# Kernel tuning notes

Hardware: AMD Instinct MI355X
Metric: run time of the kernel (lower is better)

Reference implementation:

```python
import jax, jax.numpy as jnp
import numpy as np
from jax.scipy.special import logsumexp


def _mixture_log_cdf(x, pi, mu, s):
    # x: [B,C,H,W]; pi,mu,s: [B,C,H,W,K]. log CDF of mixture of logistics.
    z = (x[..., None] - mu) * jnp.exp(-s)
    return logsumexp(jax.nn.log_softmax(pi, axis=-1) + jax.nn.log_sigmoid(z), axis=-1)


def _mixture_log_pdf(x, pi, mu, s):
    z = (x[..., None] - mu) * jnp.exp(-s)
    log_p = z - s - 2.0 * jax.nn.softplus(z)  # logistic log-density per component
    return logsumexp(jax.nn.log_softmax(pi, axis=-1) + log_p, axis=-1)


def setup_inputs() -> dict:
    key = jax.random.key(0)
    ks = jax.random.split(key, 8)
    B, C, H, W, K = 32, 8, 64, 64, 16
    shp = (B, C, H, W)
    mshp = (B, C, H, W, K)
    return {
        "x_change": jax.random.normal(ks[0], shp, jnp.float32),
        "x_id": jax.random.normal(ks[1], shp, jnp.float32),
        "sldj": jnp.zeros((B,), jnp.float32),
        "a": 0.1 * jax.random.normal(ks[2], shp, jnp.float32),
        "b": 0.1 * jax.random.normal(ks[3], shp, jnp.float32),
        "pi": jax.random.normal(ks[4], mshp, jnp.float32),
        "mu": jax.random.normal(ks[5], mshp, jnp.float32),
        "s": 0.1 * jax.random.normal(ks[6], mshp, jnp.float32),
    }


def reference(x_change, x_id, sldj, a, b, pi, mu, s):
    B = x_change.shape[0]
    # forward (reverse=False) Flow++ MixLogCDF coupling
    log_cdf = _mixture_log_cdf(x_change, pi, mu, s)  # [B,C,H,W], values <= 0
    u = jnp.exp(log_cdf)                             # CDF in (0,1)
    # sigmoid inverse (logit) with log-det: z = log(u) - log(1-u); ldj = -log(u) - log(1-u)
    out = log_cdf - jnp.log1p(-u)
    scale_ldj = -log_cdf - jnp.log1p(-u)
    out = (out + b) * jnp.exp(a)
    logistic_ldj = _mixture_log_pdf(x_change, pi, mu, s)
    sldj = sldj + jnp.sum((logistic_ldj + scale_ldj + a).reshape(B, -1), axis=-1)
    return out, x_id, sldj
```

## Files before the change

kernel.cpp:

```cpp
#include <hip/hip_runtime.h>
#include <math.h>

#define KCOMP 16
#define CHW 32768

__global__ void init_sldj_kernel(const float* __restrict__ sldj,
                                 float* __restrict__ out_sldj, int B) {
    int i = blockIdx.x * blockDim.x + threadIdx.x;
    if (i < B) out_sldj[i] = sldj[i];
}

__global__ __launch_bounds__(256) void coupling_kernel(
    const float* __restrict__ x_change, const float* __restrict__ x_id,
    const float* __restrict__ a, const float* __restrict__ b,
    const float* __restrict__ pi, const float* __restrict__ mu,
    const float* __restrict__ s, float* __restrict__ out, int N) {
    const int i = blockIdx.x * blockDim.x + threadIdx.x;
    float ldj_term = 0.0f;
    if (i < N) {
        const float x = x_change[i];

        float p[KCOMP], m[KCOMP], sv[KCOMP];
        const size_t base = (size_t)i * KCOMP;
        const float4* pv = (const float4*)(pi + base);
        const float4* mv = (const float4*)(mu + base);
        const float4* svv = (const float4*)(s + base);
#pragma unroll
        for (int c = 0; c < 4; ++c) {
            float4 t0 = pv[c];
            p[4 * c + 0] = t0.x; p[4 * c + 1] = t0.y; p[4 * c + 2] = t0.z; p[4 * c + 3] = t0.w;
            float4 t1 = mv[c];
            m[4 * c + 0] = t1.x; m[4 * c + 1] = t1.y; m[4 * c + 2] = t1.z; m[4 * c + 3] = t1.w;
            float4 t2 = svv[c];
            sv[4 * c + 0] = t2.x; sv[4 * c + 1] = t2.y; sv[4 * c + 2] = t2.z; sv[4 * c + 3] = t2.w;
        }

        float pmax = p[0];
#pragma unroll
        for (int k = 1; k < KCOMP; ++k) pmax = fmaxf(pmax, p[k]);
        float psum = 0.0f;
#pragma unroll
        for (int k = 0; k < KCOMP; ++k) psum += __expf(p[k] - pmax);
        const float lse_pi = pmax + __logf(psum);

        float t[KCOMP], q[KCOMP];
        float mt = -1e30f, mq = -1e30f;
#pragma unroll
        for (int k = 0; k < KCOMP; ++k) {
            const float lp = p[k] - lse_pi;
            const float sk = sv[k];
            const float z = (x - m[k]) * __expf(-sk);
            const float az = fabsf(z);
            const float l1 = __logf(1.0f + __expf(-az));
            const float ls = fminf(z, 0.0f) - l1;
            const float sp = fmaxf(z, 0.0f) + l1;
            const float logp = z - sk - 2.0f * sp;
            t[k] = lp + ls;
            q[k] = lp + logp;
            mt = fmaxf(mt, t[k]);
            mq = fmaxf(mq, q[k]);
        }
        float st = 0.0f, sq = 0.0f;
#pragma unroll
        for (int k = 0; k < KCOMP; ++k) {
            st += __expf(t[k] - mt);
            sq += __expf(q[k] - mq);
        }
        const float log_cdf = mt + __logf(st);
        const float logistic_ldj = mq + __logf(sq);

        float one_m_u = -expm1f(log_cdf);
        one_m_u = fmaxf(one_m_u, 1e-30f);
        const float l1mu = __logf(one_m_u);
        const float outv = log_cdf - l1mu;
        const float scale_ldj = -log_cdf - l1mu;

        const float av = a[i];
        const float bv = b[i];
        out[i] = (outv + bv) * __expf(av);
        out[(size_t)N + i] = x_id[i];
        ldj_term = logistic_ldj + scale_ldj + av;
    }

    float v = ldj_term;
#pragma unroll
    for (int off = 32; off > 0; off >>= 1) v += __shfl_down(v, off);
    __shared__ float ws[4];
    const int lane = threadIdx.x & 63;
    const int wid = threadIdx.x >> 6;
    if (lane == 0) ws[wid] = v;
    __syncthreads();
    if (threadIdx.x == 0) {
        const float tot = ws[0] + ws[1] + ws[2] + ws[3];
        const int batch = (blockIdx.x * blockDim.x) / CHW;
        atomicAdd(out + 2 * (size_t)N + batch, tot);
    }
}

extern "C" void kernel_launch(void* const* d_in, const int* in_sizes, int n_in,
                              void* d_out, int out_size, void* d_ws, size_t ws_size,
                              hipStream_t stream) {
    const float* x_change = (const float*)d_in[0];
    const float* x_id     = (const float*)d_in[1];
    const float* sldj     = (const float*)d_in[2];
    const float* a        = (const float*)d_in[3];
    const float* b        = (const float*)d_in[4];
    const float* pi       = (const float*)d_in[5];
    const float* mu       = (const float*)d_in[6];
    const float* s        = (const float*)d_in[7];
    float* out = (float*)d_out;

    const int N = in_sizes[0];
    const int B = in_sizes[2];

    init_sldj_kernel<<<1, 64, 0, stream>>>(sldj, out + 2 * (size_t)N, B);

    const int block = 256;
    const int grid = (N + block - 1) / block;
    coupling_kernel<<<grid, block, 0, stream>>>(x_change, x_id, a, b, pi, mu, s, out, N);
}
```

Baseline: 223.2 us.

## Split mixture components across 4 lanes and use linear-space CDF/PDF sums

```diff
diff --git a/kernel.cpp b/kernel.cpp
--- a/kernel.cpp
+++ b/kernel.cpp
@@ -1,8 +1,10 @@
 #include <hip/hip_runtime.h>
 #include <math.h>
 
-#define KCOMP 16
 #define CHW 32768
+#define NELEM 1048576
+#define NBLOCKS 2048
+#define CHUNKS_PER_BLOCK 8
 
 __global__ void init_sldj_kernel(const float* __restrict__ sldj,
                                  float* __restrict__ out_sldj, int B) {
@@ -10,90 +12,77 @@
     if (i < B) out_sldj[i] = sldj[i];
 }
 
-__global__ __launch_bounds__(256) void coupling_kernel(
+__global__ __launch_bounds__(256, 8) void coupling_kernel(
     const float* __restrict__ x_change, const float* __restrict__ x_id,
     const float* __restrict__ a, const float* __restrict__ b,
-    const float* __restrict__ pi, const float* __restrict__ mu,
-    const float* __restrict__ s, float* __restrict__ out, int N) {
-    const int i = blockIdx.x * blockDim.x + threadIdx.x;
-    float ldj_term = 0.0f;
-    if (i < N) {
-        const float x = x_change[i];
+    const float4* __restrict__ pi4, const float4* __restrict__ mu4,
+    const float4* __restrict__ s4, float* __restrict__ out) {
+    const int t = threadIdx.x;
+    const int kq = t & 3;
+    const int grp = t >> 2;
+    float ldj_acc = 0.0f;
 
-        float p[KCOMP], m[KCOMP], sv[KCOMP];
-        const size_t base = (size_t)i * KCOMP;
-        const float4* pv = (const float4*)(pi + base);
-        const float4* mv = (const float4*)(mu + base);
-        const float4* svv = (const float4*)(s + base);
+    for (int it = 0; it < CHUNKS_PER_BLOCK; ++it) {
+        const int chunk = blockIdx.x * CHUNKS_PER_BLOCK + it;
+        const int e = chunk * 64 + grp;
+        const size_t fi = (size_t)e * 4 + kq;
+
+        const float4 p = pi4[fi];
+        const float4 m = mu4[fi];
+        const float4 sv = s4[fi];
+        const float x = x_change[e];
+
+        float pmax = fmaxf(fmaxf(p.x, p.y), fmaxf(p.z, p.w));
+        pmax = fmaxf(pmax, __shfl_xor(pmax, 1));
+        pmax = fmaxf(pmax, __shfl_xor(pmax, 2));
+
+        float psum = 0.0f, cdf = 0.0f, pdf = 0.0f;
+        {
+            const float pk[4] = {p.x, p.y, p.z, p.w};
+            const float mk[4] = {m.x, m.y, m.z, m.w};
+            const float sk[4] = {sv.x, sv.y, sv.z, sv.w};
 #pragma unroll
-        for (int c = 0; c < 4; ++c) {
-            float4 t0 = pv[c];
-            p[4 * c + 0] = t0.x; p[4 * c + 1] = t0.y; p[4 * c + 2] = t0.z; p[4 * c + 3] = t0.w;
-            float4 t1 = mv[c];
-            m[4 * c + 0] = t1.x; m[4 * c + 1] = t1.y; m[4 * c + 2] = t1.z; m[4 * c + 3] = t1.w;
-            float4 t2 = svv[c];
-            sv[4 * c + 0] = t2.x; sv[4 * c + 1] = t2.y; sv[4 * c + 2] = t2.z; sv[4 * c + 3] = t2.w;
+            for (int j = 0; j < 4; ++j) {
+                const float w = __expf(pk[j] - pmax);
+                const float ez = __expf(-sk[j]);
+                const float z = (x - mk[j]) * ez;
+                const float g = __builtin_amdgcn_rcpf(1.0f + __expf(-z));
+                psum += w;
+                cdf += w * g;
+                pdf += w * ez * g * (1.0f - g);
+            }
         }
+        psum += __shfl_xor(psum, 1); psum += __shfl_xor(psum, 2);
+        cdf  += __shfl_xor(cdf, 1);  cdf  += __shfl_xor(cdf, 2);
+        pdf  += __shfl_xor(pdf, 1);  pdf  += __shfl_xor(pdf, 2);
 
-        float pmax = p[0];
-#pragma unroll
-        for (int k = 1; k < KCOMP; ++k) pmax = fmaxf(pmax, p[k]);
-        float psum = 0.0f;
-#pragma unroll
-        for (int k = 0; k < KCOMP; ++k) psum += __expf(p[k] - pmax);
-        const float lse_pi = pmax + __logf(psum);
-
-        float t[KCOMP], q[KCOMP];
-        float mt = -1e30f, mq = -1e30f;
-#pragma unroll
-        for (int k = 0; k < KCOMP; ++k) {
-            const float lp = p[k] - lse_pi;
-            const float sk = sv[k];
-            const float z = (x - m[k]) * __expf(-sk);
-            const float az = fabsf(z);
-            const float l1 = __logf(1.0f + __expf(-az));
-            const float ls = fminf(z, 0.0f) - l1;
-            const float sp = fmaxf(z, 0.0f) + l1;
-            const float logp = z - sk - 2.0f * sp;
-            t[k] = lp + ls;
-            q[k] = lp + logp;
-            mt = fmaxf(mt, t[k]);
-            mq = fmaxf(mq, q[k]);
+        if (kq == 0) {
+            const float lpsum = __logf(psum);
+            const float log_cdf = __logf(cdf) - lpsum;
+            const float logistic_ldj = __logf(pdf) - lpsum;
+            float omu = -expm1f(log_cdf);
+            omu = fmaxf(omu, 1e-38f);
+            const float l1mu = __logf(omu);
+            const float av = a[e];
+            const float bv = b[e];
+            out[e] = (log_cdf - l1mu + bv) * __expf(av);
+            ldj_acc += logistic_ldj - log_cdf - l1mu + av;
+        } else if (kq == 1) {
+            out[(size_t)NELEM + e] = x_id[e];
         }
-        float st = 0.0f, sq = 0.0f;
-#pragma unroll
-        for (int k = 0; k < KCOMP; ++k) {
-            st += __expf(t[k] - mt);
-            sq += __expf(q[k] - mq);
-        }
-        const float log_cdf = mt + __logf(st);
-        const float logistic_ldj = mq + __logf(sq);
-
-        float one_m_u = -expm1f(log_cdf);
-        one_m_u = fmaxf(one_m_u, 1e-30f);
-        const float l1mu = __logf(one_m_u);
-        const float outv = log_cdf - l1mu;
-        const float scale_ldj = -log_cdf - l1mu;
-
-        const float av = a[i];
-        const float bv = b[i];
-        out[i] = (outv + bv) * __expf(av);
-        out[(size_t)N + i] = x_id[i];
-        ldj_term = logistic_ldj + scale_ldj + av;
     }
 
-    float v = ldj_term;
+    float v = ldj_acc;
 #pragma unroll
     for (int off = 32; off > 0; off >>= 1) v += __shfl_down(v, off);
     __shared__ float ws[4];
-    const int lane = threadIdx.x & 63;
     const int wid = threadIdx.x >> 6;
-    if (lane == 0) ws[wid] = v;
+    if ((threadIdx.x & 63) == 0) ws[wid] = v;
     __syncthreads();
     if (threadIdx.x == 0) {
         const float tot = ws[0] + ws[1] + ws[2] + ws[3];
-        const int batch = (blockIdx.x * blockDim.x) / CHW;
-        atomicAdd(out + 2 * (size_t)N + batch, tot);
+        const int batch = blockIdx.x >> 6;
+        atomicAdd(out + 2 * (size_t)NELEM + batch, tot);
     }
 }
 
@@ -105,17 +94,14 @@
     const float* sldj     = (const float*)d_in[2];
     const float* a        = (const float*)d_in[3];
     const float* b        = (const float*)d_in[4];
-    const float* pi       = (const float*)d_in[5];
-    const float* mu       = (const float*)d_in[6];
-    const float* s        = (const float*)d_in[7];
+    const float4* pi      = (const float4*)d_in[5];
+    const float4* mu      = (const float4*)d_in[6];
+    const float4* s       = (const float4*)d_in[7];
     float* out = (float*)d_out;
 
-    const int N = in_sizes[0];
     const int B = in_sizes[2];
 
-    init_sldj_kernel<<<1, 64, 0, stream>>>(sldj, out + 2 * (size_t)N, B);
+    init_sldj_kernel<<<1, 64, 0, stream>>>(sldj, out + 2 * (size_t)NELEM, B);
 
-    const int block = 256;
-    const int grid = (N + block - 1) / block;
-    coupling_kernel<<<grid, block, 0, stream>>>(x_change, x_id, a, b, pi, mu, s, out, N);
+    coupling_kernel<<<NBLOCKS, 256, 0, stream>>>(x_change, x_id, a, b, pi, mu, s, out);
 }
```

Result: no change. 225.8 us (+1.1%).

## Compute mixture CDF and PDF in linear space with native exp2/log2

Applied to the files above, without the earlier changes.

```diff
diff --git a/kernel.cpp b/kernel.cpp
--- a/kernel.cpp
+++ b/kernel.cpp
@@ -3,6 +3,8 @@
 
 #define KCOMP 16
 #define CHW 32768
+#define LOG2E 1.44269504088896340736f
+#define LN2   0.69314718055994530942f
 
 __global__ void init_sldj_kernel(const float* __restrict__ sldj,
                                  float* __restrict__ out_sldj, int B) {
@@ -19,76 +21,77 @@
     float ldj_term = 0.0f;
     if (i < N) {
         const float x = x_change[i];
+        const size_t base = (size_t)i * KCOMP;
 
-        float p[KCOMP], m[KCOMP], sv[KCOMP];
-        const size_t base = (size_t)i * KCOMP;
-        const float4* pv = (const float4*)(pi + base);
-        const float4* mv = (const float4*)(mu + base);
-        const float4* svv = (const float4*)(s + base);
+        float p[KCOMP];
+        {
+            const float4* pv = (const float4*)(pi + base);
 #pragma unroll
-        for (int c = 0; c < 4; ++c) {
-            float4 t0 = pv[c];
-            p[4 * c + 0] = t0.x; p[4 * c + 1] = t0.y; p[4 * c + 2] = t0.z; p[4 * c + 3] = t0.w;
-            float4 t1 = mv[c];
-            m[4 * c + 0] = t1.x; m[4 * c + 1] = t1.y; m[4 * c + 2] = t1.z; m[4 * c + 3] = t1.w;
-            float4 t2 = svv[c];
-            sv[4 * c + 0] = t2.x; sv[4 * c + 1] = t2.y; sv[4 * c + 2] = t2.z; sv[4 * c + 3] = t2.w;
+            for (int c = 0; c < 4; ++c) {
+                float4 t0 = pv[c];
+                p[4 * c + 0] = t0.x; p[4 * c + 1] = t0.y;
+                p[4 * c + 2] = t0.z; p[4 * c + 3] = t0.w;
+            }
         }
-
         float pmax = p[0];
 #pragma unroll
         for (int k = 1; k < KCOMP; ++k) pmax = fmaxf(pmax, p[k]);
+
+        float w[KCOMP];
         float psum = 0.0f;
 #pragma unroll
-        for (int k = 0; k < KCOMP; ++k) psum += __expf(p[k] - pmax);
-        const float lse_pi = pmax + __logf(psum);
+        for (int k = 0; k < KCOMP; ++k) {
+            w[k] = __builtin_amdgcn_exp2f((p[k] - pmax) * LOG2E);
+            psum += w[k];
+        }
 
-        float t[KCOMP], q[KCOMP];
-        float mt = -1e30f, mq = -1e30f;
+        float m[KCOMP], sv[KCOMP];
+        {
+            const float4* mv = (const float4*)(mu + base);
+            const float4* svv = (const float4*)(s + base);
+#pragma unroll
+            for (int c = 0; c < 4; ++c) {
+                float4 t1 = mv[c];
+                m[4 * c + 0] = t1.x; m[4 * c + 1] = t1.y;
+                m[4 * c + 2] = t1.z; m[4 * c + 3] = t1.w;
+                float4 t2 = svv[c];
+                sv[4 * c + 0] = t2.x; sv[4 * c + 1] = t2.y;
+                sv[4 * c + 2] = t2.z; sv[4 * c + 3] = t2.w;
+            }
+        }
+
+        float cdf = 0.0f, omu = 0.0f, pdf = 0.0f;
 #pragma unroll
         for (int k = 0; k < KCOMP; ++k) {
-            const float lp = p[k] - lse_pi;
-            const float sk = sv[k];
-            const float z = (x - m[k]) * __expf(-sk);
-            const float az = fabsf(z);
-            const float l1 = __logf(1.0f + __expf(-az));
-            const float ls = fminf(z, 0.0f) - l1;
-            const float sp = fmaxf(z, 0.0f) + l1;
-            const float logp = z - sk - 2.0f * sp;
-            t[k] = lp + ls;
-            q[k] = lp + logp;
-            mt = fmaxf(mt, t[k]);
-            mq = fmaxf(mq, q[k]);
+            const float ez = __builtin_amdgcn_exp2f(-sv[k] * LOG2E);
+            const float z = (x - m[k]) * ez;
+            const float enz = __builtin_amdgcn_exp2f(-z * LOG2E);
+            const float g = __builtin_amdgcn_rcpf(1.0f + enz);
+            const float wg = w[k] * g;
+            cdf += wg;
+            omu += wg * enz;
+            pdf += w[k] * ez * g * g * enz;
         }
-        float st = 0.0f, sq = 0.0f;
-#pragma unroll
-        for (int k = 0; k < KCOMP; ++k) {
-            st += __expf(t[k] - mt);
-            sq += __expf(q[k] - mq);
-        }
-        const float log_cdf = mt + __logf(st);
-        const float logistic_ldj = mq + __logf(sq);
 
-        float one_m_u = -expm1f(log_cdf);
-        one_m_u = fmaxf(one_m_u, 1e-30f);
-        const float l1mu = __logf(one_m_u);
-        const float outv = log_cdf - l1mu;
-        const float scale_ldj = -log_cdf - l1mu;
+        const float l2psum = __builtin_amdgcn_logf(psum);
+        const float l2cdf  = __builtin_amdgcn_logf(cdf);
+        const float l2omu  = __builtin_amdgcn_logf(fmaxf(omu, 1e-38f));
+        const float l2pdf  = __builtin_amdgcn_logf(fmaxf(pdf, 1e-38f));
 
         const float av = a[i];
         const float bv = b[i];
-        out[i] = (outv + bv) * __expf(av);
+        const float outv = (l2cdf - l2omu) * LN2;
+        out[i] = (outv + bv) * __builtin_amdgcn_exp2f(av * LOG2E);
         out[(size_t)N + i] = x_id[i];
-        ldj_term = logistic_ldj + scale_ldj + av;
+        ldj_term = (l2pdf + l2psum - l2cdf - l2omu) * LN2 + av;
     }
 
     float v = ldj_term;
 #pragma unroll
     for (int off = 32; off > 0; off >>= 1) v += __shfl_down(v, off);
     __shared__ float ws[4];
-    const int lane = threadIdx.x & 63;
     const int wid = threadIdx.x >> 6;
-    if (lane == 0) ws[wid] = v;
+    if ((threadIdx.x & 63) == 0) ws[wid] = v;
     __syncthreads();
     if (threadIdx.x == 0) {
         const float tot = ws[0] + ws[1] + ws[2] + ws[3];
```

New measurement: 222.7 us. No clear change (-0.3%).
